# Kernel optimization log

Measured on AMD Instinct MI355X. Metric: run time of the kernel, lower is better.

## Reference

```python
import jax, jax.numpy as jnp
import numpy as np

B = 8192
HID = 1024
VD = 1024
NH = 16
DH = HID // NH  # 64
TOPK = 8
LN_EPS = 1e-5


def setup_inputs() -> dict:
    key = jax.random.key(0)
    ks = jax.random.split(key, 10)
    s = 1.0 / np.sqrt(HID)
    return {
        "hidden_state": jax.random.normal(ks[0], (B, HID), dtype=jnp.float32),
        "memory_keys": jax.random.normal(ks[1], (B, TOPK, HID), dtype=jnp.float32),
        "memory_values": jax.random.normal(ks[2], (B, TOPK, VD), dtype=jnp.float32),
        "Wq": jax.random.normal(ks[3], (HID, HID), dtype=jnp.float32) * s,
        "Wk": jax.random.normal(ks[4], (HID, HID), dtype=jnp.float32) * s,
        "Wv": jax.random.normal(ks[5], (VD, HID), dtype=jnp.float32) * s,
        "Wo": jax.random.normal(ks[6], (HID, HID), dtype=jnp.float32) * s,
        "Wg": jax.random.normal(ks[7], (2 * HID, HID), dtype=jnp.float32) * s,
        "bg": jnp.zeros((HID,), dtype=jnp.float32),
        "ln_g": jnp.ones((HID,), dtype=jnp.float32),
        "ln_b": jnp.zeros((HID,), dtype=jnp.float32),
    }


def reference(hidden_state, memory_keys, memory_values, Wq, Wk, Wv, Wo, Wg, bg, ln_g, ln_b):
    b = hidden_state.shape[0]
    scale = DH ** -0.5
    # QKV projections, reshaped into heads
    Q = (hidden_state @ Wq).reshape(b, NH, DH)          # (B, H, D)
    K = (memory_keys @ Wk).reshape(b, TOPK, NH, DH)     # (B, K, H, D)
    V = (memory_values @ Wv).reshape(b, TOPK, NH, DH)   # (B, K, H, D)
    # attention over top_k memory slots (query length 1)
    scores = jnp.einsum("bhd,bkhd->bhk", Q, K) * scale  # (B, H, K)
    attn = jax.nn.softmax(scores, axis=-1)
    out = jnp.einsum("bhk,bkhd->bhd", attn, V).reshape(b, HID)
    memory_out = out @ Wo
    # gated residual
    gate_in = jnp.concatenate([hidden_state, memory_out], axis=-1)
    g = jax.nn.sigmoid(gate_in @ Wg + bg)
    aug = hidden_state + g * memory_out
    # LayerNorm (affine, eps=1e-5)
    mean = jnp.mean(aug, axis=-1, keepdims=True)
    var = jnp.var(aug, axis=-1, keepdims=True)
    return (aug - mean) * jax.lax.rsqrt(var + LN_EPS) * ln_g + ln_b
```

## Files before the change

### kernel.cpp

```cpp
#include <hip/hip_runtime.h>
#include <hip/hip_bf16.h>

typedef __bf16 bf16;
typedef __bf16 bf16x8 __attribute__((ext_vector_type(8)));
typedef __bf16 bf16x4 __attribute__((ext_vector_type(4)));
typedef float  f32x4  __attribute__((ext_vector_type(4)));

__device__ __forceinline__ void block_barrier()
{
    asm volatile("s_waitcnt lgkmcnt(0)\n\ts_barrier" ::: "memory");
}

#if defined(__has_builtin)
#if __has_builtin(__builtin_amdgcn_global_load_lds)
#define HAS_GLD 1
#endif
#endif
#ifndef HAS_GLD
#define HAS_GLD 0
#endif

__device__ __forceinline__ void gld_lds16(const bf16* g, bf16* lds_base)
{
#if HAS_GLD
    __builtin_amdgcn_global_load_lds(
        (const __attribute__((address_space(1))) void*)g,
        (__attribute__((address_space(3))) void*)lds_base, 16, 0, 0);
#else
    *(bf16x8*)(lds_base + (threadIdx.x & 63) * 8) = *(const bf16x8*)g;
#endif
}

__global__ __launch_bounds__(256)
void transpose_cvt(const float* __restrict__ src, bf16* __restrict__ dst, int K, int N)
{
    __shared__ float t[32][33];
    const int bx = blockIdx.x, by = blockIdx.y, tid = threadIdx.x;
    const int c = tid & 31, r0 = tid >> 5;
#pragma unroll
    for (int p = 0; p < 4; p++) {
        int r = r0 + p * 8;
        t[r][c] = src[(size_t)(by * 32 + r) * N + bx * 32 + c];
    }
    __syncthreads();
#pragma unroll
    for (int p = 0; p < 4; p++) {
        int r = r0 + p * 8;
        dst[(size_t)(bx * 32 + r) * K + by * 32 + c] = (bf16)t[c][r];
    }
}

__global__ __launch_bounds__(256)
void cvt_bf16(const float* __restrict__ src, bf16* __restrict__ dst, int n8)
{
    const int i = blockIdx.x * 256 + threadIdx.x;
    if (i >= n8) return;
    const float4* s = (const float4*)(src + (size_t)i * 8);
    float4 a = s[0], b = s[1];
    bf16x8 o;
    o[0] = (bf16)a.x; o[1] = (bf16)a.y; o[2] = (bf16)a.z; o[3] = (bf16)a.w;
    o[4] = (bf16)b.x; o[5] = (bf16)b.y; o[6] = (bf16)b.z; o[7] = (bf16)b.w;
    *(bf16x8*)(dst + (size_t)i * 8) = o;
}

__global__ __launch_bounds__(256)
void repack_wv(const bf16* __restrict__ Wvt, bf16* __restrict__ Wvf)
{
    const int t = blockIdx.x * 256 + threadIdx.x;
    const int lane = t & 63, g = t >> 6;
    const int dt = g & 3, sp = (g >> 2) & 31, h = g >> 7;
    const int lm = lane & 15, q = lane >> 4;
    const bf16x8 v = *(const bf16x8*)(Wvt + (size_t)(h * 64 + dt * 16 + lm) * 1024
                                      + sp * 32 + q * 8);
    *(bf16x8*)(Wvf + (size_t)g * 512 + lane * 8) = v;
}

__global__ __launch_bounds__(256)
void repack_q(const bf16* __restrict__ Qb, bf16* __restrict__ Qf)
{
    const int t = blockIdx.x * 256 + threadIdx.x;
    const int lane = t & 63, g = t >> 6;
    const int half = g & 1, h = (g >> 1) & 15, bt = g >> 5;
    const int lm = lane & 15, q = lane >> 4;
    const bf16x8 v = *(const bf16x8*)(Qb + (size_t)(bt * 16 + lm) * 1024
                                      + h * 64 + half * 32 + q * 8);
    *(bf16x8*)(Qf + (size_t)g * 512 + lane * 8) = v;
}

__global__ __launch_bounds__(256)
void repack_wk(const bf16* __restrict__ Wkb, bf16* __restrict__ Wkf)
{
    const int t = blockIdx.x * 256 + threadIdx.x;
    const int lane = t & 63, g = t >> 6;
    const int half = g & 1, mt = (g >> 1) & 3, h = (g >> 3) & 15, c = g >> 7;
    const int lm = lane & 15, q = lane >> 4;
    const bf16x8 v = *(const bf16x8*)(Wkb + (size_t)(c * 64 + mt * 16 + lm) * 1024
                                      + h * 64 + half * 32 + q * 8);
    *(bf16x8*)(Wkf + (size_t)g * 512 + lane * 8) = v;
}

template<bool TWOA>
__global__ __launch_bounds__(256)
void gemm_a97(const bf16* __restrict__ A1, const bf16* __restrict__ A2,
              const bf16* __restrict__ Bt, float* __restrict__ Cf,
              bf16* __restrict__ Cb, int Kloop, int Ksplit,
              int ldA, int ldA2, int ldB, int ldC,
              long az, long bz, long cz)
{
    __shared__ bf16 Al[128 * 32];
    __shared__ bf16 Bl[128 * 32];

    const int z = blockIdx.z;
    A1 += (size_t)z * az;
    Bt += (size_t)z * bz;
    if (Cf) Cf += (size_t)z * cz;
    if (Cb) Cb += (size_t)z * cz;

    int bx, by;
    {
        const int gy = gridDim.y;
        const int flat = blockIdx.y * gridDim.x + blockIdx.x;
        if ((gy & 7) == 0 && gridDim.x == 8) {
            const int xcd = flat & 7, slot = flat >> 3, mpx = gy >> 3;
            by = xcd * mpx + (slot >> 3);
            bx = slot & 7;
        } else { bx = blockIdx.x; by = blockIdx.y; }
    }

    const int tid = threadIdx.x;
    const int wave = tid >> 6, lane = tid & 63;
    const int m0 = by * 128, n0 = bx * 128;
    const int rl = lane >> 2;
    const int kc = (lane & 3) * 8;
    const int wm = wave >> 1, wn = wave & 1, lm = lane & 15, quad = lane >> 4;

    f32x4 acc[4][4];
#pragma unroll
    for (int i = 0; i < 4; i++)
#pragma unroll
        for (int j = 0; j < 4; j++)
#pragma unroll
            for (int r = 0; r < 4; r++) acc[i][j][r] = 0.f;

    for (int k0 = 0; k0 < Kloop; k0 += 32) {
        const bf16* Ab; int kof, ld;
        if (TWOA && k0 >= Ksplit) { Ab = A2; kof = k0 - Ksplit; ld = ldA2; }
        else                      { Ab = A1; kof = k0;          ld = ldA;  }
        const int r0 = wave * 32 + rl, r1 = r0 + 16;
        gld_lds16(Ab + (size_t)(m0 + r0) * ld + kof + kc, Al + (wave * 32) * 32);
        gld_lds16(Ab + (size_t)(m0 + r1) * ld + kof + kc, Al + (wave * 32 + 16) * 32);
        gld_lds16(Bt + (size_t)(n0 + r0) * ldB + k0 + kc, Bl + (wave * 32) * 32);
        gld_lds16(Bt + (size_t)(n0 + r1) * ldB + k0 + kc, Bl + (wave * 32 + 16) * 32);
        __syncthreads();

        bf16x8 af[4], bfr[4];
#pragma unroll
        for (int i = 0; i < 4; i++)
            af[i] = *(const bf16x8*)&Al[(wm * 64 + i * 16 + lm) * 32 + quad * 8];
#pragma unroll
        for (int j = 0; j < 4; j++)
            bfr[j] = *(const bf16x8*)&Bl[(wn * 64 + j * 16 + lm) * 32 + quad * 8];
#pragma unroll
        for (int i = 0; i < 4; i++)
#pragma unroll
            for (int j = 0; j < 4; j++)
                acc[i][j] = __builtin_amdgcn_mfma_f32_16x16x32_bf16(af[i], bfr[j], acc[i][j], 0, 0, 0);
        __syncthreads();
    }

#pragma unroll
    for (int i = 0; i < 4; i++) {
        const int rbase = m0 + wm * 64 + i * 16 + quad * 4;
#pragma unroll
        for (int j = 0; j < 4; j++) {
            const int c = n0 + wn * 64 + j * 16 + lm;
#pragma unroll
            for (int r = 0; r < 4; r++) {
                const float v = acc[i][j][r];
                const size_t idx = (size_t)(rbase + r) * ldC + c;
                if (Cf) Cf[idx] = v;
                if (Cb) Cb[idx] = (bf16)v;
            }
        }
    }
}

__global__ __launch_bounds__(512, 4)
void score_attn_part(const bf16* __restrict__ Qf, const bf16* __restrict__ Wkf,
                     const float* __restrict__ mk, float* __restrict__ part)
{
    __shared__ bf16  Ul[16 * 1024];
    __shared__ float Ml[8 * 1024];

    const int tid  = threadIdx.x;
    const int wave = tid >> 6, lane = tid & 63;
    const int lm = lane & 15, q = lane >> 4;
    const int g  = blockIdx.x;
    const int c  = blockIdx.y;
    const int i0 = c * 64;
    const int h0 = wave * 2;

    bf16x8 wk[2][4][2];
#pragma unroll
    for (int hh = 0; hh < 2; hh++)
#pragma unroll
        for (int mt = 0; mt < 4; mt++)
#pragma unroll
            for (int half = 0; half < 2; half++)
                wk[hh][mt][half] = *(const bf16x8*)(Wkf +
                    (size_t)((((c * 16 + h0 + hh) * 4 + mt) * 2 + half)) * 512 + lane * 8);

    const int choff = lane >> 4, lli = (lane & 15) * 4;

    float* pbase = part + ((size_t)c << 20);

    int bt = g * 8;
    bf16x8 qf[2][2];
#pragma unroll
    for (int hh = 0; hh < 2; hh++)
#pragma unroll
        for (int half = 0; half < 2; half++)
            qf[hh][half] = *(const bf16x8*)(Qf +
                (size_t)(((bt * 16 + h0 + hh) * 2 + half)) * 512 + lane * 8);
#pragma unroll
    for (int s = 0; s < 4; s++) {
        const int chunk = s * 4 + choff;
        gld_lds16((const bf16*)(mk + (size_t)(bt * 16 + 2 * wave + (chunk >> 3)) * 8192
                                + (chunk & 7) * 1024 + i0 + lli),
                  (bf16*)&Ml[wave * 1024 + s * 256]);
    }

    for (int t = 0; t < 8; ++t) {
        const int b0 = g * 128 + t * 16;
        const int btn = (t < 7) ? bt + 1 : bt;

        asm volatile("s_waitcnt vmcnt(0)" ::: "memory");
        __builtin_amdgcn_sched_barrier(0);

        bf16x8 mbr[2][2];
#pragma unroll
        for (int lb = 0; lb < 2; lb++) {
            const int base = wave * 1024 + (lb * 8 + (lm & 7)) * 64;
            const f32x4 a0 = *(const f32x4*)&Ml[base + q * 8];
            const f32x4 a1 = *(const f32x4*)&Ml[base + q * 8 + 4];
            const f32x4 b0v = *(const f32x4*)&Ml[base + 32 + q * 8];
            const f32x4 b1v = *(const f32x4*)&Ml[base + 32 + q * 8 + 4];
            bf16x8 m0, m1;
            m0[0] = (bf16)a0[0]; m0[1] = (bf16)a0[1]; m0[2] = (bf16)a0[2]; m0[3] = (bf16)a0[3];
            m0[4] = (bf16)a1[0]; m0[5] = (bf16)a1[1]; m0[6] = (bf16)a1[2]; m0[7] = (bf16)a1[3];
            m1[0] = (bf16)b0v[0]; m1[1] = (bf16)b0v[1]; m1[2] = (bf16)b0v[2]; m1[3] = (bf16)b0v[3];
            m1[4] = (bf16)b1v[0]; m1[5] = (bf16)b1v[1]; m1[6] = (bf16)b1v[2]; m1[7] = (bf16)b1v[3];
            mbr[lb][0] = m0; mbr[lb][1] = m1;
        }
        asm volatile("s_waitcnt lgkmcnt(0)" ::: "memory");
        __builtin_amdgcn_sched_barrier(0);

#pragma unroll
        for (int hh = 0; hh < 2; hh++) {
            const int h = h0 + hh;
#pragma unroll
            for (int mt = 0; mt < 4; mt++) {
                f32x4 c4;
                c4[0] = 0.f; c4[1] = 0.f; c4[2] = 0.f; c4[3] = 0.f;
                c4 = __builtin_amdgcn_mfma_f32_16x16x32_bf16(wk[hh][mt][0], qf[hh][0], c4, 0, 0, 0);
                c4 = __builtin_amdgcn_mfma_f32_16x16x32_bf16(wk[hh][mt][1], qf[hh][1], c4, 0, 0, 0);
                bf16x4 o;
                o[0] = (bf16)c4[0]; o[1] = (bf16)c4[1]; o[2] = (bf16)c4[2]; o[3] = (bf16)c4[3];
                *(bf16x4*)((char*)Ul + ((((lm * 16 + h) * 64 + mt * 16 + q * 4) * 2)
                                        ^ (((lm ^ h) & 7) << 4))) = o;
            }
        }

#pragma unroll
        for (int hh = 0; hh < 2; hh++)
#pragma unroll
            for (int half = 0; half < 2; half++)
                qf[hh][half] = *(const bf16x8*)(Qf +
                    (size_t)(((btn * 16 + h0 + hh) * 2 + half)) * 512 + lane * 8);
#pragma unroll
        for (int s = 0; s < 4; s++) {
            const int chunk = s * 4 + choff;
            gld_lds16((const bf16*)(mk + (size_t)(btn * 16 + 2 * wave + (chunk >> 3)) * 8192
                                    + (chunk & 7) * 1024 + i0 + lli),
                      (bf16*)&Ml[wave * 1024 + s * 256]);
        }

        block_barrier();

#pragma unroll
        for (int lb = 0; lb < 2; lb++) {
            const int bb = wave * 2 + lb;
            const bf16x8 ua0 = *(const bf16x8*)((char*)Ul +
                ((((bb * 16 + lm) * 64 + q * 8) * 2) ^ (((bb ^ lm) & 7) << 4)));
            const bf16x8 ua1 = *(const bf16x8*)((char*)Ul +
                ((((bb * 16 + lm) * 64 + 32 + q * 8) * 2) ^ (((bb ^ lm) & 7) << 4)));

            f32x4 s4;
            s4[0] = 0.f; s4[1] = 0.f; s4[2] = 0.f; s4[3] = 0.f;
            s4 = __builtin_amdgcn_mfma_f32_16x16x32_bf16(ua0, mbr[lb][0], s4, 0, 0, 0);
            s4 = __builtin_amdgcn_mfma_f32_16x16x32_bf16(ua1, mbr[lb][1], s4, 0, 0, 0);

            if (lm < 8) {
                float* pp = pbase + (size_t)(b0 + bb) * 128 + lm;
#pragma unroll
                for (int r = 0; r < 4; r++) pp[(q * 4 + r) * 8] = s4[r];
            }
        }
        block_barrier();

        bt = btn;
    }
}

__global__ __launch_bounds__(256)
void reduce_softmax(const float* __restrict__ part, float* __restrict__ attn)
{
    const int t = blockIdx.x * 256 + threadIdx.x;
    const float* p = part + (size_t)t * 8;
    float s[8] = {0.f, 0.f, 0.f, 0.f, 0.f, 0.f, 0.f, 0.f};
#pragma unroll
    for (int c = 0; c < 16; ++c) {
        const f32x4 a = *(const f32x4*)(p + ((size_t)c << 20));
        const f32x4 b = *(const f32x4*)(p + ((size_t)c << 20) + 4);
        s[0] += a[0]; s[1] += a[1]; s[2] += a[2]; s[3] += a[3];
        s[4] += b[0]; s[5] += b[1]; s[6] += b[2]; s[7] += b[3];
    }
#pragma unroll
    for (int k = 0; k < 8; k++) s[k] *= 0.125f;
    float mx = s[0];
#pragma unroll
    for (int k = 1; k < 8; k++) mx = fmaxf(mx, s[k]);
    float den = 0.f;
#pragma unroll
    for (int k = 0; k < 8; k++) { s[k] = __expf(s[k] - mx); den += s[k]; }
    const float inv = 1.f / den;
    f32x4 o0, o1;
    o0[0] = s[0] * inv; o0[1] = s[1] * inv; o0[2] = s[2] * inv; o0[3] = s[3] * inv;
    o1[0] = s[4] * inv; o1[1] = s[5] * inv; o1[2] = s[6] * inv; o1[3] = s[7] * inv;
    *(f32x4*)(attn + (size_t)t * 8)     = o0;
    *(f32x4*)(attn + (size_t)t * 8 + 4) = o1;
}

__global__ __launch_bounds__(512, 4)
void apply_attn(const float* __restrict__ attn, const float* __restrict__ mv,
                const bf16* __restrict__ Wvf, bf16* __restrict__ OH)
{
    __shared__ float Vl32[3][4096];
    __shared__ bf16  Wl[16 * 16 * 32];

    const int tid  = threadIdx.x;
    const int wave = tid >> 6, lane = tid & 63;
    const int lm = lane & 15, q = lane >> 4;
    const int b0 = blockIdx.x * 16;
    const int h0 = wave * 2;

    const int gk = lane >> 3, gi4 = (lane & 7) * 4;

    bf16x8 afv[2][2];
#pragma unroll
    for (int lb = 0; lb < 2; lb++) {
        const float* ap = attn + (size_t)(b0 + wave * 2 + lb) * 128 + lm * 8;
        const float4 x = *(const float4*)(ap);
        const float4 y = *(const float4*)(ap + 4);
        bf16 a8[8];
        a8[0] = (bf16)x.x; a8[1] = (bf16)x.y; a8[2] = (bf16)x.z; a8[3] = (bf16)x.w;
        a8[4] = (bf16)y.x; a8[5] = (bf16)y.y; a8[6] = (bf16)y.z; a8[7] = (bf16)y.w;
#pragma unroll
        for (int mt = 0; mt < 2; mt++) {
            bf16x8 t;
#pragma unroll
            for (int j = 0; j < 8; j++) t[j] = (q == mt) ? a8[j] : (bf16)0.f;
            afv[lb][mt] = t;
        }
    }

    f32x4 oacc[2][4];
#pragma unroll
    for (int i = 0; i < 2; i++)
#pragma unroll
        for (int j = 0; j < 4; j++)
#pragma unroll
            for (int r = 0; r < 4; r++) oacc[i][j][r] = 0.f;

#pragma unroll
    for (int m = 0; m < 2; m++) {
        const int row = 2 * wave + m;
        gld_lds16((const bf16*)(mv + (size_t)(b0 + row) * 8192 + gk * 1024 + gi4),
                  (bf16*)&Vl32[0][row * 256]);
    }
#pragma unroll
    for (int m = 0; m < 2; m++) {
        const int row = 2 * wave + m;
        gld_lds16((const bf16*)(mv + (size_t)(b0 + row) * 8192 + gk * 1024 + 32 + gi4),
                  (bf16*)&Vl32[1][row * 256]);
    }

    for (int sp = 0; sp < 32; ++sp) {
        const int ni = (sp + 2 < 32) ? sp * 32 + 64 : 0;
        const int cb = sp % 3, nb = (sp + 2) % 3;

        bf16x8 wb[2][4];
#pragma unroll
        for (int hh = 0; hh < 2; hh++) {
            const int h = h0 + hh;
#pragma unroll
            for (int dt = 0; dt < 4; dt++)
                wb[hh][dt] = *(const bf16x8*)(Wvf +
                    ((((size_t)h * 32 + sp) * 4 + dt) * 512 + lane * 8));
        }
        __builtin_amdgcn_sched_barrier(0);

#pragma unroll
        for (int m = 0; m < 2; m++) {
            const int row = 2 * wave + m;
            gld_lds16((const bf16*)(mv + (size_t)(b0 + row) * 8192 + gk * 1024 + ni + gi4),
                      (bf16*)&Vl32[nb][row * 256]);
        }
        __builtin_amdgcn_sched_barrier(0);

        asm volatile("s_waitcnt vmcnt(12)" ::: "memory");
        __builtin_amdgcn_sched_barrier(0);
#pragma unroll
        for (int lb = 0; lb < 2; lb++) {
            const int row = 2 * wave + lb;
            const int il = (q & 1) * 16 + lm;
            float v[8];
#pragma unroll
            for (int k = 0; k < 8; k++) v[k] = Vl32[cb][row * 256 + k * 32 + il];
            bf16x8 avf;
#pragma unroll
            for (int k = 0; k < 8; k++) avf[k] = (bf16)v[k];
#pragma unroll
            for (int mt = 0; mt < 2; mt++) {
                f32x4 c;
                c[0] = 0.f; c[1] = 0.f; c[2] = 0.f; c[3] = 0.f;
                c = __builtin_amdgcn_mfma_f32_16x16x32_bf16(avf, afv[lb][mt], c, 0, 0, 0);
                bf16x4 o;
                o[0] = (bf16)c[0]; o[1] = (bf16)c[1]; o[2] = (bf16)c[2]; o[3] = (bf16)c[3];
                *(bf16x4*)((char*)Wl + ((((row * 16 + lm) * 32 + mt * 16 + q * 4) * 2)
                                        ^ (((row ^ lm) & 7) << 4))) = o;
            }
        }
        block_barrier();

        asm volatile("s_waitcnt vmcnt(2)" ::: "memory");
        __builtin_amdgcn_sched_barrier(0);
#pragma unroll
        for (int hh = 0; hh < 2; hh++) {
            const int h = h0 + hh;
            const bf16x8 wa = *(const bf16x8*)((char*)Wl +
                ((((lm * 16 + h) * 32 + q * 8) * 2) ^ (((lm ^ h) & 7) << 4)));
#pragma unroll
            for (int dt = 0; dt < 4; dt++)
                oacc[hh][dt] = __builtin_amdgcn_mfma_f32_16x16x32_bf16(wa, wb[hh][dt], oacc[hh][dt], 0, 0, 0);
        }
        block_barrier();
    }

#pragma unroll
    for (int hh = 0; hh < 2; hh++) {
        const int h = h0 + hh;
#pragma unroll
        for (int dt = 0; dt < 4; dt++) {
#pragma unroll
            for (int r = 0; r < 4; r++)
                OH[(size_t)(b0 + q * 4 + r) * 1024 + h * 64 + dt * 16 + lm] = (bf16)oacc[hh][dt][r];
        }
    }
}

__global__ __launch_bounds__(256)
void gate_ln_kernel(const float* __restrict__ hs, const float* __restrict__ mo,
                    const float* __restrict__ z,  const float* __restrict__ bg,
                    const float* __restrict__ lng, const float* __restrict__ lnb,
                    float* __restrict__ out)
{
    __shared__ float s1[4], s2[4];
    const int tid = threadIdx.x;
    const size_t base = (size_t)blockIdx.x * 1024 + tid * 4;

    const float4 h4 = *(const float4*)&hs[base];
    const float4 m4 = *(const float4*)&mo[base];
    const float4 z4 = *(const float4*)&z[base];
    const float4 bg4 = *(const float4*)&bg[tid * 4];

    float a[4];
    {
        const float g0 = 1.f / (1.f + __expf(-(z4.x + bg4.x)));
        const float g1 = 1.f / (1.f + __expf(-(z4.y + bg4.y)));
        const float g2 = 1.f / (1.f + __expf(-(z4.z + bg4.z)));
        const float g3 = 1.f / (1.f + __expf(-(z4.w + bg4.w)));
        a[0] = h4.x + g0 * m4.x;
        a[1] = h4.y + g1 * m4.y;
        a[2] = h4.z + g2 * m4.z;
        a[3] = h4.w + g3 * m4.w;
    }
    float sum = a[0] + a[1] + a[2] + a[3];
    float sq  = a[0]*a[0] + a[1]*a[1] + a[2]*a[2] + a[3]*a[3];
#pragma unroll
    for (int off = 32; off >= 1; off >>= 1) {
        sum += __shfl_xor(sum, off);
        sq  += __shfl_xor(sq,  off);
    }
    const int wave = tid >> 6;
    if ((tid & 63) == 0) { s1[wave] = sum; s2[wave] = sq; }
    __syncthreads();
    const float mean = (s1[0] + s1[1] + s1[2] + s1[3]) * (1.f / 1024.f);
    const float var  = (s2[0] + s2[1] + s2[2] + s2[3]) * (1.f / 1024.f) - mean * mean;
    const float inv  = rsqrtf(var + 1e-5f);

    const float4 g4 = *(const float4*)&lng[tid * 4];
    const float4 b4 = *(const float4*)&lnb[tid * 4];
    float4 o;
    o.x = (a[0] - mean) * inv * g4.x + b4.x;
    o.y = (a[1] - mean) * inv * g4.y + b4.y;
    o.z = (a[2] - mean) * inv * g4.z + b4.z;
    o.w = (a[3] - mean) * inv * g4.w + b4.w;
    *(float4*)&out[base] = o;
}

extern "C" void kernel_launch(void* const* d_in, const int* in_sizes, int n_in,
                              void* d_out, int out_size, void* d_ws, size_t ws_size,
                              hipStream_t stream)
{
    const float* hs  = (const float*)d_in[0];
    const float* mk  = (const float*)d_in[1];
    const float* mv  = (const float*)d_in[2];
    const float* Wq  = (const float*)d_in[3];
    const float* Wk  = (const float*)d_in[4];
    const float* Wv  = (const float*)d_in[5];
    const float* Wo  = (const float*)d_in[6];
    const float* Wg  = (const float*)d_in[7];
    const float* bg  = (const float*)d_in[8];
    const float* lng = (const float*)d_in[9];
    const float* lnb = (const float*)d_in[10];
    float* out = (float*)d_out;

    const int B = 8192;
    const dim3 tb(256);

    char* ws = (char*)d_ws;
    bf16*  Wq_t = (bf16*)(ws);
    bf16*  Wv_t = (bf16*)(ws + ((size_t)2  << 20));
    bf16*  Wo_t = (bf16*)(ws + ((size_t)4  << 20));
    bf16*  Wg_t = (bf16*)(ws + ((size_t)6  << 20));
    bf16*  Wk_b = (bf16*)(ws + ((size_t)10 << 20));
    bf16*  hs_b = (bf16*)(ws + ((size_t)12 << 20));
    bf16*  Qb   = (bf16*)(ws + ((size_t)28 << 20));
    bf16*  OH   = (bf16*)(ws + ((size_t)44 << 20));
    float* Mo   = (float*)(ws + ((size_t)60 << 20));
    bf16*  Mo_b = (bf16*)(ws + ((size_t)92 << 20));
    float* Zb   = (float*)(ws + ((size_t)108 << 20));
    float* At   = (float*)(ws + ((size_t)140 << 20));
    float* Atp  = (float*)(ws + ((size_t)144 << 20));
    bf16*  Wvf  = (bf16*)(ws + ((size_t)208 << 20));
    bf16*  Wkf  = (bf16*)(ws + ((size_t)210 << 20));
    bf16*  Qf   = (bf16*)(ws + ((size_t)212 << 20));

    transpose_cvt<<<dim3(32, 32), tb, 0, stream>>>(Wq, Wq_t, 1024, 1024);
    transpose_cvt<<<dim3(32, 32), tb, 0, stream>>>(Wv, Wv_t, 1024, 1024);
    transpose_cvt<<<dim3(32, 32), tb, 0, stream>>>(Wo, Wo_t, 1024, 1024);
    transpose_cvt<<<dim3(32, 64), tb, 0, stream>>>(Wg, Wg_t, 2048, 1024);
    cvt_bf16<<<dim3(1024 * 1024 / 8 / 256), tb, 0, stream>>>(Wk, Wk_b, 1024 * 1024 / 8);
    cvt_bf16<<<dim3(B * 1024 / 8 / 256), tb, 0, stream>>>(hs, hs_b, B * 1024 / 8);
    repack_wv<<<dim3(512), tb, 0, stream>>>(Wv_t, Wvf);
    repack_wk<<<dim3(512), tb, 0, stream>>>(Wk_b, Wkf);

    gemm_a97<false><<<dim3(8, 64, 1), tb, 0, stream>>>(
        hs_b, nullptr, Wq_t, nullptr, Qb,
        1024, 1024, 1024, 0, 1024, 1024, 0, 0, 0);
    repack_q<<<dim3(4096), tb, 0, stream>>>(Qb, Qf);
    score_attn_part<<<dim3(64, 16), dim3(512), 0, stream>>>(Qf, Wkf, mk, Atp);
    reduce_softmax<<<dim3(512), tb, 0, stream>>>(Atp, At);
    apply_attn<<<dim3(B / 16), dim3(512), 0, stream>>>(At, mv, Wvf, OH);
    gemm_a97<false><<<dim3(8, 64, 1), tb, 0, stream>>>(
        OH, nullptr, Wo_t, Mo, Mo_b,
        1024, 1024, 1024, 0, 1024, 1024, 0, 0, 0);
    gemm_a97<true><<<dim3(8, 64, 1), tb, 0, stream>>>(
        hs_b, Mo_b, Wg_t, Zb, nullptr,
        2048, 1024, 1024, 1024, 2048, 1024, 0, 0, 0);
    gate_ln_kernel<<<dim3(B), tb, 0, stream>>>(
        hs, Mo, Zb, bg, lng, lnb, out);
}
```

Measured before the change: 452.4 us.

## Fuse score computation across full K with softmax, removing split-K partial buffers

The score kernel no longer splits the key dimension across 16 blocks writing partial scores to a large workspace. Each block now loops over all 32 K slices, streaming memory keys through a double-buffered LDS tile and accumulating scores in MFMA registers. The softmax is then applied in-kernel with lane shuffles, so the separate reduce_softmax kernel and its launch go away. This removes the large partial-score write and read-back traffic. In exchange, each block reloads Wk fragments from cache on every slice instead of keeping them in registers, and the Wk repack layout changes to match.

```diff
diff --git a/kernel.cpp b/kernel.cpp
--- a/kernel.cpp
+++ b/kernel.cpp
@@ -88,13 +88,13 @@
 }
 
 __global__ __launch_bounds__(256)
-void repack_wk(const bf16* __restrict__ Wkb, bf16* __restrict__ Wkf)
+void repack_wk2(const bf16* __restrict__ Wkb, bf16* __restrict__ Wkf)
 {
     const int t = blockIdx.x * 256 + threadIdx.x;
     const int lane = t & 63, g = t >> 6;
-    const int half = g & 1, mt = (g >> 1) & 3, h = (g >> 3) & 15, c = g >> 7;
+    const int half = g & 1, h = (g >> 1) & 15, mt = (g >> 5) & 1, sp = g >> 6;
     const int lm = lane & 15, q = lane >> 4;
-    const bf16x8 v = *(const bf16x8*)(Wkb + (size_t)(c * 64 + mt * 16 + lm) * 1024
+    const bf16x8 v = *(const bf16x8*)(Wkb + (size_t)(sp * 32 + mt * 16 + lm) * 1024
                                       + h * 64 + half * 32 + q * 8);
     *(bf16x8*)(Wkf + (size_t)g * 512 + lane * 8) = v;
 }
@@ -186,159 +186,122 @@
 }
 
 __global__ __launch_bounds__(512, 4)
-void score_attn_part(const bf16* __restrict__ Qf, const bf16* __restrict__ Wkf,
-                     const float* __restrict__ mk, float* __restrict__ part)
-{
-    __shared__ bf16  Ul[16 * 1024];
-    __shared__ float Ml[8 * 1024];
+void score_attn(const bf16* __restrict__ Qf, const bf16* __restrict__ Wkf,
+                const float* __restrict__ mk, float* __restrict__ attn)
+{
+    __shared__ bf16  Ul[16 * 16 * 32];
+    __shared__ float Ml[2][4096];
 
     const int tid  = threadIdx.x;
     const int wave = tid >> 6, lane = tid & 63;
     const int lm = lane & 15, q = lane >> 4;
-    const int g  = blockIdx.x;
-    const int c  = blockIdx.y;
-    const int i0 = c * 64;
+    const int bt = blockIdx.x;
     const int h0 = wave * 2;
 
-    bf16x8 wk[2][4][2];
-#pragma unroll
-    for (int hh = 0; hh < 2; hh++)
-#pragma unroll
-        for (int mt = 0; mt < 4; mt++)
-#pragma unroll
-            for (int half = 0; half < 2; half++)
-                wk[hh][mt][half] = *(const bf16x8*)(Wkf +
-                    (size_t)((((c * 16 + h0 + hh) * 4 + mt) * 2 + half)) * 512 + lane * 8);
-
-    const int choff = lane >> 4, lli = (lane & 15) * 4;
-
-    float* pbase = part + ((size_t)c << 20);
-
-    int bt = g * 8;
+    const int gk = lane & 7, gg4 = lane >> 3;
+
     bf16x8 qf[2][2];
 #pragma unroll
     for (int hh = 0; hh < 2; hh++)
 #pragma unroll
         for (int half = 0; half < 2; half++)
             qf[hh][half] = *(const bf16x8*)(Qf +
-                (size_t)(((bt * 16 + h0 + hh) * 2 + half)) * 512 + lane * 8);
-#pragma unroll
-    for (int s = 0; s < 4; s++) {
-        const int chunk = s * 4 + choff;
-        gld_lds16((const bf16*)(mk + (size_t)(bt * 16 + 2 * wave + (chunk >> 3)) * 8192
-                                + (chunk & 7) * 1024 + i0 + lli),
-                  (bf16*)&Ml[wave * 1024 + s * 256]);
-    }
-
-    for (int t = 0; t < 8; ++t) {
-        const int b0 = g * 128 + t * 16;
-        const int btn = (t < 7) ? bt + 1 : bt;
-
-        asm volatile("s_waitcnt vmcnt(0)" ::: "memory");
-        __builtin_amdgcn_sched_barrier(0);
-
-        bf16x8 mbr[2][2];
-#pragma unroll
-        for (int lb = 0; lb < 2; lb++) {
-            const int base = wave * 1024 + (lb * 8 + (lm & 7)) * 64;
-            const f32x4 a0 = *(const f32x4*)&Ml[base + q * 8];
-            const f32x4 a1 = *(const f32x4*)&Ml[base + q * 8 + 4];
-            const f32x4 b0v = *(const f32x4*)&Ml[base + 32 + q * 8];
-            const f32x4 b1v = *(const f32x4*)&Ml[base + 32 + q * 8 + 4];
-            bf16x8 m0, m1;
-            m0[0] = (bf16)a0[0]; m0[1] = (bf16)a0[1]; m0[2] = (bf16)a0[2]; m0[3] = (bf16)a0[3];
-            m0[4] = (bf16)a1[0]; m0[5] = (bf16)a1[1]; m0[6] = (bf16)a1[2]; m0[7] = (bf16)a1[3];
-            m1[0] = (bf16)b0v[0]; m1[1] = (bf16)b0v[1]; m1[2] = (bf16)b0v[2]; m1[3] = (bf16)b0v[3];
-            m1[4] = (bf16)b1v[0]; m1[5] = (bf16)b1v[1]; m1[6] = (bf16)b1v[2]; m1[7] = (bf16)b1v[3];
-            mbr[lb][0] = m0; mbr[lb][1] = m1;
-        }
-        asm volatile("s_waitcnt lgkmcnt(0)" ::: "memory");
-        __builtin_amdgcn_sched_barrier(0);
-
+                (size_t)((bt * 16 + h0 + hh) * 2 + half) * 512 + lane * 8);
+
+    f32x4 sacc[2];
+#pragma unroll
+    for (int lb = 0; lb < 2; lb++)
+#pragma unroll
+        for (int r = 0; r < 4; r++) sacc[lb][r] = 0.f;
+
+#pragma unroll
+    for (int m = 0; m < 2; m++) {
+        const int row = 2 * wave + m;
+        gld_lds16((const bf16*)(mk + (size_t)(bt * 16 + row) * 8192 + gk * 1024 + gg4 * 4),
+                  (bf16*)&Ml[0][row * 256]);
+    }
+
+    for (int sp = 0; sp < 32; ++sp) {
+        const int ni = (sp + 1 < 32) ? (sp + 1) * 32 : 0;
+        const int cb = sp & 1, nb = cb ^ 1;
+
+        bf16x8 wk[2][2][2];
+#pragma unroll
+        for (int hh = 0; hh < 2; hh++)
+#pragma unroll
+            for (int mt = 0; mt < 2; mt++)
+#pragma unroll
+                for (int half = 0; half < 2; half++)
+                    wk[hh][mt][half] = *(const bf16x8*)(Wkf +
+                        (size_t)(((sp * 2 + mt) * 16 + h0 + hh) * 2 + half) * 512 + lane * 8);
+        __builtin_amdgcn_sched_barrier(0);
+
+#pragma unroll
+        for (int m = 0; m < 2; m++) {
+            const int row = 2 * wave + m;
+            gld_lds16((const bf16*)(mk + (size_t)(bt * 16 + row) * 8192 + gk * 1024 + ni + gg4 * 4),
+                      (bf16*)&Ml[nb][row * 256]);
+        }
+        __builtin_amdgcn_sched_barrier(0);
+
+        asm volatile("s_waitcnt vmcnt(2)" ::: "memory");
+        __builtin_amdgcn_sched_barrier(0);
 #pragma unroll
         for (int hh = 0; hh < 2; hh++) {
             const int h = h0 + hh;
 #pragma unroll
-            for (int mt = 0; mt < 4; mt++) {
+            for (int mt = 0; mt < 2; mt++) {
                 f32x4 c4;
                 c4[0] = 0.f; c4[1] = 0.f; c4[2] = 0.f; c4[3] = 0.f;
                 c4 = __builtin_amdgcn_mfma_f32_16x16x32_bf16(wk[hh][mt][0], qf[hh][0], c4, 0, 0, 0);
                 c4 = __builtin_amdgcn_mfma_f32_16x16x32_bf16(wk[hh][mt][1], qf[hh][1], c4, 0, 0, 0);
                 bf16x4 o;
                 o[0] = (bf16)c4[0]; o[1] = (bf16)c4[1]; o[2] = (bf16)c4[2]; o[3] = (bf16)c4[3];
-                *(bf16x4*)((char*)Ul + ((((lm * 16 + h) * 64 + mt * 16 + q * 4) * 2)
+                *(bf16x4*)((char*)Ul + ((((lm * 16 + h) * 32 + mt * 16 + q * 4) * 2)
                                         ^ (((lm ^ h) & 7) << 4))) = o;
             }
         }
-
-#pragma unroll
-        for (int hh = 0; hh < 2; hh++)
-#pragma unroll
-            for (int half = 0; half < 2; half++)
-                qf[hh][half] = *(const bf16x8*)(Qf +
-                    (size_t)(((btn * 16 + h0 + hh) * 2 + half)) * 512 + lane * 8);
-#pragma unroll
-        for (int s = 0; s < 4; s++) {
-            const int chunk = s * 4 + choff;
-            gld_lds16((const bf16*)(mk + (size_t)(btn * 16 + 2 * wave + (chunk >> 3)) * 8192
-                                    + (chunk & 7) * 1024 + i0 + lli),
-                      (bf16*)&Ml[wave * 1024 + s * 256]);
-        }
-
         block_barrier();
 
 #pragma unroll
         for (int lb = 0; lb < 2; lb++) {
             const int bb = wave * 2 + lb;
-            const bf16x8 ua0 = *(const bf16x8*)((char*)Ul +
-                ((((bb * 16 + lm) * 64 + q * 8) * 2) ^ (((bb ^ lm) & 7) << 4)));
-            const bf16x8 ua1 = *(const bf16x8*)((char*)Ul +
-                ((((bb * 16 + lm) * 64 + 32 + q * 8) * 2) ^ (((bb ^ lm) & 7) << 4)));
-
-            f32x4 s4;
-            s4[0] = 0.f; s4[1] = 0.f; s4[2] = 0.f; s4[3] = 0.f;
-            s4 = __builtin_amdgcn_mfma_f32_16x16x32_bf16(ua0, mbr[lb][0], s4, 0, 0, 0);
-            s4 = __builtin_amdgcn_mfma_f32_16x16x32_bf16(ua1, mbr[lb][1], s4, 0, 0, 0);
-
-            if (lm < 8) {
-                float* pp = pbase + (size_t)(b0 + bb) * 128 + lm;
-#pragma unroll
-                for (int r = 0; r < 4; r++) pp[(q * 4 + r) * 8] = s4[r];
-            }
+            const bf16x8 ua = *(const bf16x8*)((char*)Ul +
+                ((((bb * 16 + lm) * 32 + q * 8) * 2) ^ (((bb ^ lm) & 7) << 4)));
+            const int mbase = bb * 256 + (lane & 7) * 4;
+            (void)mbase;
+            const int kk = lm & 7;
+            const f32x4 a0 = *(const f32x4*)&Ml[cb][bb * 256 + (q * 2) * 32 + kk * 4];
+            const f32x4 a1 = *(const f32x4*)&Ml[cb][bb * 256 + (q * 2 + 1) * 32 + kk * 4];
+            bf16x8 mb;
+            mb[0] = (bf16)a0[0]; mb[1] = (bf16)a0[1]; mb[2] = (bf16)a0[2]; mb[3] = (bf16)a0[3];
+            mb[4] = (bf16)a1[0]; mb[5] = (bf16)a1[1]; mb[6] = (bf16)a1[2]; mb[7] = (bf16)a1[3];
+            sacc[lb] = __builtin_amdgcn_mfma_f32_16x16x32_bf16(ua, mb, sacc[lb], 0, 0, 0);
         }
         block_barrier();
-
-        bt = btn;
-    }
-}
-
-__global__ __launch_bounds__(256)
-void reduce_softmax(const float* __restrict__ part, float* __restrict__ attn)
-{
-    const int t = blockIdx.x * 256 + threadIdx.x;
-    const float* p = part + (size_t)t * 8;
-    float s[8] = {0.f, 0.f, 0.f, 0.f, 0.f, 0.f, 0.f, 0.f};
-#pragma unroll
-    for (int c = 0; c < 16; ++c) {
-        const f32x4 a = *(const f32x4*)(p + ((size_t)c << 20));
-        const f32x4 b = *(const f32x4*)(p + ((size_t)c << 20) + 4);
-        s[0] += a[0]; s[1] += a[1]; s[2] += a[2]; s[3] += a[3];
-        s[4] += b[0]; s[5] += b[1]; s[6] += b[2]; s[7] += b[3];
-    }
-#pragma unroll
-    for (int k = 0; k < 8; k++) s[k] *= 0.125f;
-    float mx = s[0];
-#pragma unroll
-    for (int k = 1; k < 8; k++) mx = fmaxf(mx, s[k]);
-    float den = 0.f;
-#pragma unroll
-    for (int k = 0; k < 8; k++) { s[k] = __expf(s[k] - mx); den += s[k]; }
-    const float inv = 1.f / den;
-    f32x4 o0, o1;
-    o0[0] = s[0] * inv; o0[1] = s[1] * inv; o0[2] = s[2] * inv; o0[3] = s[3] * inv;
-    o1[0] = s[4] * inv; o1[1] = s[5] * inv; o1[2] = s[6] * inv; o1[3] = s[7] * inv;
-    *(f32x4*)(attn + (size_t)t * 8)     = o0;
-    *(f32x4*)(attn + (size_t)t * 8 + 4) = o1;
+    }
+
+#pragma unroll
+    for (int lb = 0; lb < 2; lb++) {
+        const size_t bb = (size_t)(bt * 16 + wave * 2 + lb);
+#pragma unroll
+        for (int r = 0; r < 4; r++) {
+            float s = sacc[lb][r] * 0.125f;
+            float mx = s;
+            mx = fmaxf(mx, __shfl_xor(mx, 1));
+            mx = fmaxf(mx, __shfl_xor(mx, 2));
+            mx = fmaxf(mx, __shfl_xor(mx, 4));
+            mx = fmaxf(mx, __shfl_xor(mx, 8));
+            const float e = __expf(s - mx);
+            float d = e;
+            d += __shfl_xor(d, 1);
+            d += __shfl_xor(d, 2);
+            d += __shfl_xor(d, 4);
+            d += __shfl_xor(d, 8);
+            const float a = e * (2.f / d);
+            if (lm < 8) attn[bb * 128 + (q * 4 + r) * 8 + lm] = a;
+        }
+    }
 }
 
 __global__ __launch_bounds__(512, 4)
@@ -552,7 +515,6 @@
     bf16*  Mo_b = (bf16*)(ws + ((size_t)92 << 20));
     float* Zb   = (float*)(ws + ((size_t)108 << 20));
     float* At   = (float*)(ws + ((size_t)140 << 20));
-    float* Atp  = (float*)(ws + ((size_t)144 << 20));
     bf16*  Wvf  = (bf16*)(ws + ((size_t)208 << 20));
     bf16*  Wkf  = (bf16*)(ws + ((size_t)210 << 20));
     bf16*  Qf   = (bf16*)(ws + ((size_t)212 << 20));
@@ -564,14 +526,13 @@
     cvt_bf16<<<dim3(1024 * 1024 / 8 / 256), tb, 0, stream>>>(Wk, Wk_b, 1024 * 1024 / 8);
     cvt_bf16<<<dim3(B * 1024 / 8 / 256), tb, 0, stream>>>(hs, hs_b, B * 1024 / 8);
     repack_wv<<<dim3(512), tb, 0, stream>>>(Wv_t, Wvf);
-    repack_wk<<<dim3(512), tb, 0, stream>>>(Wk_b, Wkf);
+    repack_wk2<<<dim3(512), tb, 0, stream>>>(Wk_b, Wkf);
 
     gemm_a97<false><<<dim3(8, 64, 1), tb, 0, stream>>>(
         hs_b, nullptr, Wq_t, nullptr, Qb,
         1024, 1024, 1024, 0, 1024, 1024, 0, 0, 0);
     repack_q<<<dim3(4096), tb, 0, stream>>>(Qb, Qf);
-    score_attn_part<<<dim3(64, 16), dim3(512), 0, stream>>>(Qf, Wkf, mk, Atp);
-    reduce_softmax<<<dim3(512), tb, 0, stream>>>(Atp, At);
+    score_attn<<<dim3(B / 16), dim3(512), 0, stream>>>(Qf, Wkf, mk, At);
     apply_attn<<<dim3(B / 16), dim3(512), 0, stream>>>(At, mv, Wvf, OH);
     gemm_a97<false><<<dim3(8, 64, 1), tb, 0, stream>>>(
         OH, nullptr, Wo_t, Mo, Mo_b,
```

Result: faster. 426.3 us (-5.8%).
